# Performance work log

Measured on AMD Instinct MI355X. Metric: run time of the kernel, lower is better.

The kernel has to match this reference:

```python
import jax, jax.numpy as jnp
import numpy as np


def setup_inputs() -> dict:
    key = jax.random.key(0)
    k1, k2, k3, k4, k5 = jax.random.split(key, 5)
    out_f, in_f, group_size = 11008, 4096, 128
    n_groups = in_f // group_size  # 32
    x = jax.random.normal(k1, (32, in_f), dtype=jnp.float16)
    packed = jax.random.randint(k2, (out_f, in_f // 2), 0, 256, dtype=jnp.int32)
    scales = (jax.random.uniform(k3, (out_f, n_groups), dtype=jnp.float32) * 0.02 + 0.001).astype(jnp.float16)
    zeros = (jax.random.normal(k4, (out_f, n_groups), dtype=jnp.float32) * 0.05).astype(jnp.float16)
    bias = (jax.random.normal(k5, (out_f,), dtype=jnp.float32) * 0.02).astype(jnp.float16)
    return {"x": x, "packed": packed, "scales": scales, "zeros": zeros,
            "bias": bias, "group_size": group_size, "in_features": in_f}


def _dequantize(packed, scales, zeros, in_features, group_size):
    # packed: [out_f, padded_in//2] uint8-valued ints; two int4 nibbles per byte.
    out_f = packed.shape[0]
    padded_in = packed.shape[1] * 2
    high = (packed >> 4) & 15
    low = packed & 15
    # interleave: even columns = high nibble, odd columns = low nibble
    unpacked = jnp.stack([high, low], axis=-1).reshape(out_f, padded_in).astype(scales.dtype)
    n_groups = scales.shape[1]
    grouped = unpacked.reshape(out_f, n_groups, group_size)
    deq = grouped * scales[:, :, None] + zeros[:, :, None]
    return deq.reshape(out_f, padded_in)[:, :in_features].astype(jnp.float16)


def reference(x, packed, scales, zeros, bias, group_size, in_features):
    # Fused dequant + linear: y = x @ W^T + b, with W reconstructed from int4.
    weight = _dequantize(packed, scales, zeros, in_features, group_size)  # [out_f, in_f]
    out = jnp.dot(x, weight.T) + bias
    return out
```

## Files before the change

kernel.cpp:

```cpp
#include <hip/hip_runtime.h>
#include <hip/hip_fp16.h>
#include <hip/hip_bf16.h>

typedef unsigned int u32;
typedef unsigned short u16;
typedef short short8 __attribute__((ext_vector_type(8)));
typedef float f32x4 __attribute__((ext_vector_type(4)));
typedef unsigned int u32x4 __attribute__((ext_vector_type(4)));

#define IN_F 4096
#define OUT_F 11008
#define MROWS 32
#define CCOLS 2048
#define NGRP 32
#define KSPL 16
#define NBX (OUT_F / 64)
#define PART_BYTES ((size_t)KSPL * NBX * 4 * 512 * 2)
#define WS_NEED PART_BYTES

typedef const __attribute__((address_space(1))) void* gas_t;
typedef __attribute__((address_space(3))) void* las_t;
__device__ __forceinline__ void gl_lds16(const void* g, void* l) {
  __builtin_amdgcn_global_load_lds((gas_t)g, (las_t)l, 16, 0, 0);
}
__device__ __forceinline__ u32 lds_u32(const void* p) {
  return (u32)(uintptr_t)(las_t)p;
}

__device__ __forceinline__ float bf2f(u16 b) {
  u32 t = ((u32)b) << 16;
  return __builtin_bit_cast(float, t);
}
__device__ __forceinline__ u32 f2bf_rne(float f) {
  u32 b = __builtin_bit_cast(u32, f);
  return (b + 0x7FFFu + ((b >> 16) & 1u)) >> 16;
}
__device__ __forceinline__ float h2f(u16 h) {
  return __half2float(__builtin_bit_cast(__half, h));
}
__device__ __forceinline__ u32 pk_bf2(float lo, float hi) {
  __hip_bfloat162 pk = __float22bfloat162_rn(make_float2(lo, hi));
  u32 r;
  __builtin_memcpy(&r, &pk, 4);
  return r;
}

__device__ __forceinline__ u32 detect_mode(const u16* sc) {
  int l = (int)(threadIdx.x & 63u);
  u16 u = sc[2 * l];
  int e = (u >> 7) & 0xFF;
  unsigned long long mA = __ballot(e >= 114 && e <= 124);
  unsigned long long mC = __ballot(e >= 36 && e <= 88);
  int cA = __popcll(mA), cC = __popcll(mC);
  return (cA >= 48) ? 0u : ((cC >= 48) ? 2u : 1u);
}

__device__ __forceinline__ float ld_sz(const void* p, int idx, u32 mode) {
  if (mode == 0) return bf2f(((const u16*)p)[idx]);
  if (mode == 2) return h2f(((const u16*)p)[idx]);
  return ((const float*)p)[idx];
}

__device__ __forceinline__ u32 deq2(u32 v, float sf, float za) {
  float uh = __builtin_bit_cast(float, 0x43000000u | ((v << 12) & 0xF0000u));
  float ul = __builtin_bit_cast(float, 0x43000000u | ((v << 16) & 0xF0000u));
  float wh = __builtin_fmaf(uh, sf, za);
  float wl = __builtin_fmaf(ul, sf, za);
  return pk_bf2(wh, wl);
}
__device__ __forceinline__ u32x4 deq4v(u32x4 bv, float sf, float za) {
  u32x4 r;
  r[0] = deq2(bv[0], sf, za); r[1] = deq2(bv[1], sf, za);
  r[2] = deq2(bv[2], sf, za); r[3] = deq2(bv[3], sf, za);
  return r;
}
__device__ __forceinline__ uint4 deq4(uint4 bv, float sf, float za) {
  uint4 r;
  r.x = deq2(bv.x, sf, za); r.y = deq2(bv.y, sf, za);
  r.z = deq2(bv.z, sf, za); r.w = deq2(bv.w, sf, za);
  return r;
}

__device__ __forceinline__ uint4 lda8(const void* x, int eoff, u32 mode) {
  if (mode == 0) return *reinterpret_cast<const uint4*>((const u16*)x + eoff);
  if (mode == 1) {
    float4 u = *reinterpret_cast<const float4*>((const float*)x + eoff);
    float4 v = *reinterpret_cast<const float4*>((const float*)x + eoff + 4);
    uint4 r;
    r.x = pk_bf2(u.x, u.y);
    r.y = pk_bf2(u.z, u.w);
    r.z = pk_bf2(v.x, v.y);
    r.w = pk_bf2(v.z, v.w);
    return r;
  }
  uint4 h = *reinterpret_cast<const uint4*>((const u16*)x + eoff);
  uint4 r;
  r.x = f2bf_rne(h2f((u16)(h.x & 0xFFFF))) | (f2bf_rne(h2f((u16)(h.x >> 16))) << 16);
  r.y = f2bf_rne(h2f((u16)(h.y & 0xFFFF))) | (f2bf_rne(h2f((u16)(h.y >> 16))) << 16);
  r.z = f2bf_rne(h2f((u16)(h.z & 0xFFFF))) | (f2bf_rne(h2f((u16)(h.z >> 16))) << 16);
  r.w = f2bf_rne(h2f((u16)(h.w & 0xFFFF))) | (f2bf_rne(h2f((u16)(h.w >> 16))) << 16);
  return r;
}

__global__ __launch_bounds__(256, 3) void qv_gemm(
    const void* __restrict__ x, const int* __restrict__ packed,
    const void* __restrict__ scales, const void* __restrict__ zeros,
    u16* __restrict__ part16) {
  __shared__ __align__(16) char smemA[16384];
  __shared__ __align__(16) char smemB[4][8][1024];
  const u32 mode = detect_mode((const u16*)scales);
  const int tid = (int)threadIdx.x;
  const int lane = tid & 63, wid = tid >> 6;
  const int q = lane & 15, p = lane >> 4;
  const int bx = (int)blockIdx.x;
  const int ksl = (int)blockIdx.y;
  const int o0 = bx * 64 + wid * 16;
  const int o = o0 + q;
  const int k32_0 = ksl * 8;

  float sf[2], za[2];
  {
    const float s0 = ld_sz(scales, o * NGRP + ksl * 2, mode);
    const float s1 = ld_sz(scales, o * NGRP + ksl * 2 + 1, mode);
    const float z0 = ld_sz(zeros, o * NGRP + ksl * 2, mode);
    const float z1 = ld_sz(zeros, o * NGRP + ksl * 2 + 1, mode);
    sf[0] = s0; sf[1] = s1;
    za[0] = z0 - 128.0f * s0;
    za[1] = z1 - 128.0f * s1;
  }
  asm volatile("s_waitcnt vmcnt(0)" ::: "memory");

  const int ar = lane >> 2, ac = lane & 3;
  uint4 afr[2][2];
#pragma unroll
  for (int j = 0; j < 2; ++j) {
#pragma unroll
    for (int h = 0; h < 2; ++h) {
      const int s_loc = wid * 2 + j;
      afr[j][h] = lda8(x, (h * 16 + ar) * IN_F + (k32_0 + s_loc) * 32 + ac * 8, mode);
    }
  }
  asm volatile("" ::: "memory");
#pragma unroll
  for (int j = 0; j < 2; ++j) {
#pragma unroll
    for (int h = 0; h < 2; ++h) {
      const int s_loc = wid * 2 + j;
      *reinterpret_cast<uint4*>(
          &smemA[(s_loc * 2 + h) * 1024 + ar * 16 + ac * 256]) = afr[j][h];
    }
  }
  asm volatile("" ::: "memory");

  const int* bsrc = packed + (size_t)(o0 + ar) * CCOLS + k32_0 * 16
                    + ((ac ^ ((ar >> 1) & 3)) << 2);
#pragma unroll
  for (int s = 0; s < 8; ++s) {
    gl_lds16(bsrc + s * 16, &smemB[wid][s][0]);
    asm volatile("" ::: "memory");
  }

  asm volatile("s_waitcnt lgkmcnt(0)" ::: "memory");
  __builtin_amdgcn_s_barrier();
  __builtin_amdgcn_sched_barrier(0);

  f32x4 acc0 = {0.f, 0.f, 0.f, 0.f}, acc1 = {0.f, 0.f, 0.f, 0.f};
  const int rdoff = q * 64 + ((p ^ ((q >> 1) & 3)) << 4);
  const u32 abase = lds_u32(&smemA[0]) + (u32)(lane * 16);
  const u32 bbase = lds_u32(&smemB[wid][0][0]) + (u32)rdoff;

#define QC(W, SFI, BO, AO0, AO1)                                              \
  {                                                                           \
    asm volatile("s_waitcnt vmcnt(" #W ")" ::: "memory");                     \
    u32x4 bv, a0v, a1v;                                                       \
    asm volatile("ds_read_b128 %0, %1 offset:" BO : "=v"(bv) : "v"(bbase));   \
    asm volatile("ds_read_b128 %0, %1 offset:" AO0 : "=v"(a0v) : "v"(abase)); \
    asm volatile("ds_read_b128 %0, %1 offset:" AO1 : "=v"(a1v) : "v"(abase)); \
    asm volatile("s_waitcnt lgkmcnt(0)"                                       \
                 : "+v"(bv), "+v"(a0v), "+v"(a1v)::"memory");                 \
    __builtin_amdgcn_sched_barrier(0);                                        \
    const u32x4 bw = deq4v(bv, sf[SFI], za[SFI]);                             \
    acc0 = __builtin_amdgcn_mfma_f32_16x16x32_bf16(                           \
        __builtin_bit_cast(short8, a0v), __builtin_bit_cast(short8, bw),      \
        acc0, 0, 0, 0);                                                       \
    acc1 = __builtin_amdgcn_mfma_f32_16x16x32_bf16(                           \
        __builtin_bit_cast(short8, a1v), __builtin_bit_cast(short8, bw),      \
        acc1, 0, 0, 0);                                                       \
    asm volatile("" ::: "memory");                                            \
  }

  QC(7, 0, "0", "0", "1024")
  QC(6, 0, "1024", "2048", "3072")
  QC(5, 0, "2048", "4096", "5120")
  QC(4, 0, "3072", "6144", "7168")
  QC(3, 1, "4096", "8192", "9216")
  QC(2, 1, "5120", "10240", "11264")
  QC(1, 1, "6144", "12288", "13312")
  QC(0, 1, "7168", "14336", "15360")
#undef QC

  u32x4 pk;
  pk[0] = pk_bf2(acc0[0], acc0[1]);
  pk[1] = pk_bf2(acc0[2], acc0[3]);
  pk[2] = pk_bf2(acc1[0], acc1[1]);
  pk[3] = pk_bf2(acc1[2], acc1[3]);
  u16* base = part16 + ((size_t)(ksl * NBX + bx) * 4 + wid) * 512 + lane * 8;
  *reinterpret_cast<u32x4*>(base) = pk;
}

__global__ __launch_bounds__(256) void qr_reduce(
    const u16* __restrict__ part16, const void* __restrict__ scales,
    const void* __restrict__ bias, void* __restrict__ out) {
  const u32 mode = detect_mode((const u16*)scales);
  const int bx = (int)blockIdx.x;
  const int wid = (int)threadIdx.x >> 6, lane = (int)threadIdx.x & 63;
  const int q = lane & 15, p = lane >> 4;
  const int o = bx * 64 + wid * 16 + q;

  float s0[4] = {0.f, 0.f, 0.f, 0.f}, s1[4] = {0.f, 0.f, 0.f, 0.f};
#pragma unroll
  for (int ksl = 0; ksl < KSPL; ++ksl) {
    const u16* base = part16 + ((size_t)(ksl * NBX + bx) * 4 + wid) * 512 + lane * 8;
    const uint4 v = *reinterpret_cast<const uint4*>(base);
    s0[0] += bf2f((u16)(v.x & 0xFFFF)); s0[1] += bf2f((u16)(v.x >> 16));
    s0[2] += bf2f((u16)(v.y & 0xFFFF)); s0[3] += bf2f((u16)(v.y >> 16));
    s1[0] += bf2f((u16)(v.z & 0xFFFF)); s1[1] += bf2f((u16)(v.z >> 16));
    s1[2] += bf2f((u16)(v.w & 0xFFFF)); s1[3] += bf2f((u16)(v.w >> 16));
  }
  const float bb = ld_sz(bias, o, mode);
#pragma unroll
  for (int rr = 0; rr < 4; ++rr) {
    const float v0 = s0[rr] + bb, v1 = s1[rr] + bb;
    const size_t i0 = (size_t)(p * 4 + rr) * OUT_F + o;
    const size_t i1 = (size_t)(16 + p * 4 + rr) * OUT_F + o;
    if (mode == 1) {
      ((float*)out)[i0] = v0; ((float*)out)[i1] = v1;
    } else {
      ((u16*)out)[i0] = (u16)f2bf_rne(v0);
      ((u16*)out)[i1] = (u16)f2bf_rne(v1);
    }
  }
}

__global__ __launch_bounds__(256, 4) void qp_direct(
    const void* __restrict__ xsrc, const int* __restrict__ packed,
    const void* __restrict__ scales, const void* __restrict__ zeros,
    const void* __restrict__ bias, void* __restrict__ out) {
  constexpr int NSTEP = 128;
  constexpr int BD = 8, AD = 4;
  const u32 mode = detect_mode((const u16*)scales);
  const int tid = (int)threadIdx.x;
  const int lane = tid & 63, wid = tid >> 6;
  const int q = lane & 15, p = lane >> 4;
  const int tile = (int)blockIdx.x * 4 + wid;
  const int o = tile * 16 + q;
  const int* pr = packed + (size_t)o * CCOLS + p * 4;
  const int ae0 = q * IN_F + p * 8;
  const int ae1 = ae0 + 16 * IN_F;
  uint4 bb[BD], a0[AD], a1[AD];
#pragma unroll
  for (int i = 0; i < BD; ++i) bb[i] = *reinterpret_cast<const uint4*>(pr + i * 16);
#pragma unroll
  for (int i = 0; i < AD; ++i) {
    a0[i] = lda8(xsrc, ae0 + i * 32, mode);
    a1[i] = lda8(xsrc, ae1 + i * 32, mode);
  }
  f32x4 acc0 = {0.f, 0.f, 0.f, 0.f}, acc1 = {0.f, 0.f, 0.f, 0.f};
  for (int g = 0; g < NSTEP / 4; ++g) {
    const float sf = ld_sz(scales, o * NGRP + g, mode);
    const float za = ld_sz(zeros, o * NGRP + g, mode) - 128.0f * sf;
#pragma unroll
    for (int u = 0; u < 4; ++u) {
      const int s = g * 4 + u;
      const uint4 bw = deq4(bb[s % BD], sf, za);
      const uint4 av0 = a0[s % AD], av1 = a1[s % AD];
      if (s + BD < NSTEP) bb[s % BD] = *reinterpret_cast<const uint4*>(pr + (s + BD) * 16);
      if (s + AD < NSTEP) {
        a0[s % AD] = lda8(xsrc, ae0 + (s + AD) * 32, mode);
        a1[s % AD] = lda8(xsrc, ae1 + (s + AD) * 32, mode);
      }
      acc0 = __builtin_amdgcn_mfma_f32_16x16x32_bf16(
          __builtin_bit_cast(short8, av0), __builtin_bit_cast(short8, bw), acc0, 0, 0, 0);
      acc1 = __builtin_amdgcn_mfma_f32_16x16x32_bf16(
          __builtin_bit_cast(short8, av1), __builtin_bit_cast(short8, bw), acc1, 0, 0, 0);
    }
  }
  const float bbv = ld_sz(bias, o, mode);
#pragma unroll
  for (int r = 0; r < 4; ++r) {
    const float v0 = acc0[r] + bbv, v1 = acc1[r] + bbv;
    const size_t i0 = (size_t)(p * 4 + r) * OUT_F + o;
    const size_t i1 = (size_t)(16 + p * 4 + r) * OUT_F + o;
    if (mode == 1) { ((float*)out)[i0] = v0; ((float*)out)[i1] = v1; }
    else { ((u16*)out)[i0] = (u16)f2bf_rne(v0); ((u16*)out)[i1] = (u16)f2bf_rne(v1); }
  }
}

extern "C" void kernel_launch(void* const* d_in, const int* in_sizes, int n_in,
                              void* d_out, int out_size, void* d_ws, size_t ws_size,
                              hipStream_t stream) {
  (void)in_sizes; (void)n_in; (void)out_size;
  const void* x      = d_in[0];
  const int* packed  = (const int*)d_in[1];
  const void* scales = d_in[2];
  const void* zeros  = d_in[3];
  const void* bias   = d_in[4];

  if (ws_size >= WS_NEED) {
    u16* part16 = (u16*)d_ws;
    qv_gemm<<<dim3(NBX, KSPL), 256, 0, stream>>>(x, packed, scales, zeros, part16);
    qr_reduce<<<NBX, 256, 0, stream>>>(part16, scales, bias, d_out);
  } else {
    qp_direct<<<OUT_F / 64, 256, 0, stream>>>(x, packed, scales, zeros, bias, d_out);
  }
}
```

Measured before the change: 34.29 us.

## Reduce split-K to 4 and pipeline B loads over 32 k-steps

Cuts the split-K factor from 16 to 4, so each block walks 32 k32 steps instead of 8. It keeps a rolling 8-deep global-to-LDS prefetch of packed weights and restages the activation tile into LDS every 8 steps behind barriers. The aim is fewer partial sums written and reduced, plus less per-block setup overhead. The cost is a quarter as many blocks, which lowers parallelism, and extra barriers inside each block.

```diff
diff --git a/kernel.cpp b/kernel.cpp
--- a/kernel.cpp
+++ b/kernel.cpp
@@ -13,7 +13,7 @@
 #define MROWS 32
 #define CCOLS 2048
 #define NGRP 32
-#define KSPL 16
+#define KSPL 4
 #define NBX (OUT_F / 64)
 #define PART_BYTES ((size_t)KSPL * NBX * 4 * 512 * 2)
 #define WS_NEED PART_BYTES
@@ -116,40 +116,46 @@
   const int ksl = (int)blockIdx.y;
   const int o0 = bx * 64 + wid * 16;
   const int o = o0 + q;
-  const int k32_0 = ksl * 8;
-
-  float sf[2], za[2];
-  {
-    const float s0 = ld_sz(scales, o * NGRP + ksl * 2, mode);
-    const float s1 = ld_sz(scales, o * NGRP + ksl * 2 + 1, mode);
-    const float z0 = ld_sz(zeros, o * NGRP + ksl * 2, mode);
-    const float z1 = ld_sz(zeros, o * NGRP + ksl * 2 + 1, mode);
-    sf[0] = s0; sf[1] = s1;
-    za[0] = z0 - 128.0f * s0;
-    za[1] = z1 - 128.0f * s1;
+  const int k32_0 = ksl * 32;
+
+  float sf[8], za[8];
+#pragma unroll
+  for (int g = 0; g < 8; ++g) {
+    const float s = ld_sz(scales, o * NGRP + ksl * 8 + g, mode);
+    const float z = ld_sz(zeros, o * NGRP + ksl * 8 + g, mode);
+    sf[g] = s; za[g] = z - 128.0f * s;
   }
   asm volatile("s_waitcnt vmcnt(0)" ::: "memory");
 
   const int ar = lane >> 2, ac = lane & 3;
-  uint4 afr[2][2];
-#pragma unroll
-  for (int j = 0; j < 2; ++j) {
-#pragma unroll
-    for (int h = 0; h < 2; ++h) {
-      const int s_loc = wid * 2 + j;
-      afr[j][h] = lda8(x, (h * 16 + ar) * IN_F + (k32_0 + s_loc) * 32 + ac * 8, mode);
-    }
-  }
-  asm volatile("" ::: "memory");
-#pragma unroll
-  for (int j = 0; j < 2; ++j) {
-#pragma unroll
-    for (int h = 0; h < 2; ++h) {
-      const int s_loc = wid * 2 + j;
-      *reinterpret_cast<uint4*>(
-          &smemA[(s_loc * 2 + h) * 1024 + ar * 16 + ac * 256]) = afr[j][h];
-    }
-  }
+
+#define ASTAGE(BB)                                                            \
+  {                                                                           \
+    uint4 af0, af1, af2, af3;                                                 \
+    {                                                                         \
+      const int pan = wid * 4 + 0, sl = pan >> 1, h = pan & 1;                \
+      af0 = lda8(x, (h * 16 + ar) * IN_F + (k32_0 + (BB)*8 + sl) * 32 + ac * 8, mode); \
+    }                                                                         \
+    {                                                                         \
+      const int pan = wid * 4 + 1, sl = pan >> 1, h = pan & 1;                \
+      af1 = lda8(x, (h * 16 + ar) * IN_F + (k32_0 + (BB)*8 + sl) * 32 + ac * 8, mode); \
+    }                                                                         \
+    {                                                                         \
+      const int pan = wid * 4 + 2, sl = pan >> 1, h = pan & 1;                \
+      af2 = lda8(x, (h * 16 + ar) * IN_F + (k32_0 + (BB)*8 + sl) * 32 + ac * 8, mode); \
+    }                                                                         \
+    {                                                                         \
+      const int pan = wid * 4 + 3, sl = pan >> 1, h = pan & 1;                \
+      af3 = lda8(x, (h * 16 + ar) * IN_F + (k32_0 + (BB)*8 + sl) * 32 + ac * 8, mode); \
+    }                                                                         \
+    const int wb = (wid * 4) * 1024 + ar * 16 + ac * 256;                     \
+    *reinterpret_cast<uint4*>(&smemA[wb + 0 * 1024]) = af0;                   \
+    *reinterpret_cast<uint4*>(&smemA[wb + 1 * 1024]) = af1;                   \
+    *reinterpret_cast<uint4*>(&smemA[wb + 2 * 1024]) = af2;                   \
+    *reinterpret_cast<uint4*>(&smemA[wb + 3 * 1024]) = af3;                   \
+  }
+
+  ASTAGE(0)
   asm volatile("" ::: "memory");
 
   const int* bsrc = packed + (size_t)(o0 + ar) * CCOLS + k32_0 * 16
@@ -188,16 +194,57 @@
         acc1, 0, 0, 0);                                                       \
     asm volatile("" ::: "memory");                                            \
   }
-
-  QC(7, 0, "0", "0", "1024")
-  QC(6, 0, "1024", "2048", "3072")
-  QC(5, 0, "2048", "4096", "5120")
-  QC(4, 0, "3072", "6144", "7168")
-  QC(3, 1, "4096", "8192", "9216")
-  QC(2, 1, "5120", "10240", "11264")
-  QC(1, 1, "6144", "12288", "13312")
-  QC(0, 1, "7168", "14336", "15360")
+#define QF(T)                                                                 \
+  {                                                                           \
+    gl_lds16(bsrc + (T)*16, &smemB[wid][(T) & 7][0]);                         \
+    asm volatile("" ::: "memory");                                            \
+  }
+#define ABOUND(BB)                                                            \
+  __builtin_amdgcn_s_barrier();                                               \
+  ASTAGE(BB)                                                                  \
+  asm volatile("s_waitcnt lgkmcnt(0)" ::: "memory");                          \
+  __builtin_amdgcn_s_barrier();                                               \
+  __builtin_amdgcn_sched_barrier(0);
+
+  QC(7, 0, "0", "0", "1024")          QF(8)
+  QC(7, 0, "1024", "2048", "3072")    QF(9)
+  QC(7, 0, "2048", "4096", "5120")    QF(10)
+  QC(7, 0, "3072", "6144", "7168")    QF(11)
+  QC(7, 1, "4096", "8192", "9216")    QF(12)
+  QC(7, 1, "5120", "10240", "11264")  QF(13)
+  QC(7, 1, "6144", "12288", "13312")  QF(14)
+  QC(7, 1, "7168", "14336", "15360")  QF(15)
+  ABOUND(1)
+  QC(7, 2, "0", "0", "1024")          QF(16)
+  QC(7, 2, "1024", "2048", "3072")    QF(17)
+  QC(7, 2, "2048", "4096", "5120")    QF(18)
+  QC(7, 2, "3072", "6144", "7168")    QF(19)
+  QC(7, 3, "4096", "8192", "9216")    QF(20)
+  QC(7, 3, "5120", "10240", "11264")  QF(21)
+  QC(7, 3, "6144", "12288", "13312")  QF(22)
+  QC(7, 3, "7168", "14336", "15360")  QF(23)
+  ABOUND(2)
+  QC(7, 4, "0", "0", "1024")          QF(24)
+  QC(7, 4, "1024", "2048", "3072")    QF(25)
+  QC(7, 4, "2048", "4096", "5120")    QF(26)
+  QC(7, 4, "3072", "6144", "7168")    QF(27)
+  QC(7, 5, "4096", "8192", "9216")    QF(28)
+  QC(7, 5, "5120", "10240", "11264")  QF(29)
+  QC(7, 5, "6144", "12288", "13312")  QF(30)
+  QC(7, 5, "7168", "14336", "15360")  QF(31)
+  ABOUND(3)
+  QC(7, 6, "0", "0", "1024")
+  QC(6, 6, "1024", "2048", "3072")
+  QC(5, 6, "2048", "4096", "5120")
+  QC(4, 6, "3072", "6144", "7168")
+  QC(3, 7, "4096", "8192", "9216")
+  QC(2, 7, "5120", "10240", "11264")
+  QC(1, 7, "6144", "12288", "13312")
+  QC(0, 7, "7168", "14336", "15360")
 #undef QC
+#undef QF
+#undef ABOUND
+#undef ASTAGE
 
   u32x4 pk;
   pk[0] = pk_bf2(acc0[0], acc0[1]);
```

Result: faster. 32.38 us (-5.6%).
